# Kernel tuning notes

Hardware: AMD Instinct MI355X
Metric: run time of the kernel (lower is better)

Reference implementation:

```python
import jax, jax.numpy as jnp
import numpy as np

FFT_BINS = 513   # win_length//2 + 1
WIN = 1024       # win_length
H = 128          # LSTM hidden size (both blocks)
ENC = 256        # encoder_size
EPS = 1e-7


def _lstm_cell(x, h, c, Wih, Whh, bih, bhh):
    # x: [1, in], h/c: [1, H]; PyTorch gate order i, f, g, o
    g = x @ Wih.T + bih + h @ Whh.T + bhh
    i, f, gg, o = jnp.split(g, 4, axis=-1)
    c2 = jax.nn.sigmoid(f) * c + jax.nn.sigmoid(i) * jnp.tanh(gg)
    h2 = jax.nn.sigmoid(o) * jnp.tanh(c2)
    return h2, c2


def _sep_block(x, states, Wih0, Whh0, bih0, bhh0, Wih1, Whh1, bih1, bhh1, dw, db):
    # x: [1,1,in]; states: [1,1,2*2*H] -> [2(h/c), 2(layers), 1, H]
    st = states.reshape(2, 2, 1, H)
    h0, c0 = st[0], st[1]
    xt = x[:, 0]                                   # [1, in]
    h1, c1 = _lstm_cell(xt, h0[0], c0[0], Wih0, Whh0, bih0, bhh0)
    h2, c2 = _lstm_cell(h1, h0[1], c0[1], Wih1, Whh1, bih1, bhh1)
    mask = jax.nn.sigmoid(h2 @ dw.T + db)[:, None, :]   # [1,1,in]
    out_states = jnp.stack([jnp.stack([h1, h2]), jnp.stack([c1, c2])]).reshape(1, 1, -1)
    return mask, out_states


def setup_inputs() -> dict:
    key = jax.random.key(0)
    ks = jax.random.split(key, 32)
    s = 0.08  # ~ 1/sqrt(H), matching PyTorch LSTM init scale
    def n(i, shape, sc=s):
        return jax.random.normal(ks[i], shape, dtype=jnp.float32) * sc
    inp = {
        "mag": jax.random.uniform(ks[0], (1, 1, FFT_BINS), dtype=jnp.float32),
        "phase": n(1, (1, 1, FFT_BINS), 3.0),
        "in_states1": n(2, (1, 1, 2 * 2 * H), 1.0),
        "in_states2": n(3, (1, 1, 2 * 2 * H), 1.0),
        # sep1 LSTM (input 513)
        "w_ih1_0": n(4, (4 * H, FFT_BINS)), "w_hh1_0": n(5, (4 * H, H)),
        "b_ih1_0": n(6, (4 * H,)), "b_hh1_0": n(7, (4 * H,)),
        "w_ih1_1": n(8, (4 * H, H)), "w_hh1_1": n(9, (4 * H, H)),
        "b_ih1_1": n(10, (4 * H,)), "b_hh1_1": n(11, (4 * H,)),
        "dense1_w": n(12, (FFT_BINS, H)), "dense1_b": n(13, (FFT_BINS,)),
        # encoder 1x1 conv (no bias) + instant layernorm
        "enc_w": n(14, (ENC, WIN)),
        "gamma": jnp.ones((1, 1, ENC), jnp.float32),
        "beta": jnp.zeros((1, 1, ENC), jnp.float32),
        # sep2 LSTM (input 256)
        "w_ih2_0": n(15, (4 * H, ENC)), "w_hh2_0": n(16, (4 * H, H)),
        "b_ih2_0": n(17, (4 * H,)), "b_hh2_0": n(18, (4 * H,)),
        "w_ih2_1": n(19, (4 * H, H)), "w_hh2_1": n(20, (4 * H, H)),
        "b_ih2_1": n(21, (4 * H,)), "b_hh2_1": n(22, (4 * H,)),
        "dense2_w": n(23, (ENC, H)), "dense2_b": n(24, (ENC,)),
        # decoder 1x1 conv (no bias)
        "dec_w": n(25, (WIN, ENC)),
    }
    return inp


def reference(mag, phase, in_states1, in_states2,
              w_ih1_0, w_hh1_0, b_ih1_0, b_hh1_0,
              w_ih1_1, w_hh1_1, b_ih1_1, b_hh1_1,
              dense1_w, dense1_b, enc_w, gamma, beta,
              w_ih2_0, w_hh2_0, b_ih2_0, b_hh2_0,
              w_ih2_1, w_hh2_1, b_ih2_1, b_hh2_1,
              dense2_w, dense2_b, dec_w):
    # Branch 1: magnitude masking in STFT domain
    mask1, out_states1 = _sep_block(mag, in_states1, w_ih1_0, w_hh1_0, b_ih1_0,
                                    b_hh1_0, w_ih1_1, w_hh1_1, b_ih1_1, b_hh1_1,
                                    dense1_w, dense1_b)
    est_mag = mask1 * mag
    s1_stft = est_mag * jnp.exp(1j * phase)          # [1,1,513] complex64
    y1 = jnp.fft.irfft(s1_stft, axis=-1)             # [1,1,1024]
    # encoder 1x1 conv (permute + conv1d(k=1) == matmul over channels)
    enc = jnp.einsum('btw,ew->bte', y1, enc_w)       # [1,1,256]
    # instant layer norm over channels
    mean = jnp.mean(enc, axis=-1, keepdims=True)
    var = jnp.mean(jnp.square(enc - mean), axis=-1, keepdims=True)
    enc_norm = (enc - mean) / jnp.sqrt(var + EPS) * gamma + beta
    # Branch 2: learned-domain masking
    mask2, out_states2 = _sep_block(enc_norm, in_states2, w_ih2_0, w_hh2_0,
                                    b_ih2_0, b_hh2_0, w_ih2_1, w_hh2_1,
                                    b_ih2_1, b_hh2_1, dense2_w, dense2_b)
    est_enc = mask2 * enc
    decoded = jnp.einsum('bte,we->bwt', est_enc, dec_w)  # [1,1024,1]
    return decoded, out_states1, out_states2
```

## Files before the change

### kernel.cpp

```cpp
#include <hip/hip_runtime.h>
#include <hip/hip_bf16.h>


#define HDIM 128
#define NB 64
typedef __hip_bfloat16 bf16;

__device__ float G[4608];
#define O_H1A 0
#define O_H2A 128
#define O_C1A 256
#define O_C2A 384
#define O_H1B 512
#define O_H2B 640
#define O_C1B 768
#define O_C2B 896
#define O_XR  1024
#define O_XI  1600
#define O_Y   2176
#define O_ENC 3200
#define O_EST 3456

__device__ unsigned bar_cnt = 0;
__device__ unsigned bar_sense = 0;

__device__ __forceinline__ void gsync() {
    __syncthreads();
    if (threadIdx.x == 0) {
        unsigned s0 = __hip_atomic_load(&bar_sense, __ATOMIC_RELAXED, __HIP_MEMORY_SCOPE_AGENT);
        unsigned old = __hip_atomic_fetch_add(&bar_cnt, 1u, __ATOMIC_RELAXED, __HIP_MEMORY_SCOPE_AGENT);
        if (old == NB - 1) {
            __hip_atomic_store(&bar_cnt, 0u, __ATOMIC_RELAXED, __HIP_MEMORY_SCOPE_AGENT);
            __hip_atomic_store(&bar_sense, s0 + 1u, __ATOMIC_RELEASE, __HIP_MEMORY_SCOPE_AGENT);
        } else {
            while (__hip_atomic_load(&bar_sense, __ATOMIC_RELAXED, __HIP_MEMORY_SCOPE_AGENT) == s0)
                __builtin_amdgcn_s_sleep(2);
        }
    }
    __syncthreads();
}

__device__ __forceinline__ void gput(int i, float v) {
    __hip_atomic_store(&G[i], v, __ATOMIC_RELAXED, __HIP_MEMORY_SCOPE_AGENT);
}
__device__ __forceinline__ float gget(int i) {
    return __hip_atomic_load(&G[i], __ATOMIC_RELAXED, __HIP_MEMORY_SCOPE_AGENT);
}

__device__ __forceinline__ bool is_bf(const void* probe) {
    return (((const unsigned*)probe)[0] & 0xFFFFu) == 0x3F80u;
}
__device__ __forceinline__ float blo(unsigned u) { return __uint_as_float(u << 16); }
__device__ __forceinline__ float bhi(unsigned u) { return __uint_as_float(u & 0xFFFF0000u); }

template <bool BF>
__device__ __forceinline__ float ld1(const void* p, int i) {
    if (BF) return __uint_as_float((unsigned)((const unsigned short*)p)[i] << 16);
    return ((const float*)p)[i];
}
template <bool BF>
__device__ __forceinline__ float2 ld2(const void* p, int i) {
    if (BF) { unsigned u = ((const unsigned*)p)[i]; return float2{blo(u), bhi(u)}; }
    return ((const float2*)p)[i];
}
template <bool BF>
__device__ __forceinline__ float4 ld4(const void* p, int i) {
    if (BF) { uint2 u = ((const uint2*)p)[i]; return float4{blo(u.x), bhi(u.x), blo(u.y), bhi(u.y)}; }
    return ((const float4*)p)[i];
}
template <bool BF>
__device__ __forceinline__ void stout(void* p, int i, float v) {
    if (BF) ((bf16*)p)[i] = __float2bfloat16(v);
    else    ((float*)p)[i] = v;
}
__device__ __forceinline__ float wred(float v) {
#pragma unroll
    for (int m = 32; m; m >>= 1) v += __shfl_xor(v, m);
    return v;
}
__device__ __forceinline__ float sigm(float x) { return 1.f / (1.f + expf(-x)); }

struct P { const void* in[28]; void* out; };

template <bool BF>
__device__ __forceinline__ void body(const P& p, float* sA, float* sB, float* sR)
{
    const int tid = threadIdx.x, lane = tid & 63, wave = tid >> 6;
    const int b = blockIdx.x;
    const int gw = b * 4 + wave;

    { float2 v = ld2<BF>(p.in[0], tid); sA[2 * tid] = v.x; sA[2 * tid + 1] = v.y; }
    if (tid == 0) sA[512] = ld1<BF>(p.in[0], 512);
    if (tid < 64) { float2 v = ld2<BF>(p.in[2], tid); sB[2 * tid] = v.x; sB[2 * tid + 1] = v.y; }
    __syncthreads();
#pragma unroll
    for (int u = 0; u < 2; ++u) {
        const int row = wave * 128 + 2 * b + u;
        float acc = 0.f;
#pragma unroll
        for (int jj = 0; jj < 9; ++jj) {
            int k = lane + 64 * jj;
            if (k < 513) acc += ld1<BF>(p.in[4], row * 513 + k) * sA[k];
        }
        { float2 w2 = ld2<BF>(p.in[5], row * 64 + lane);
          acc += w2.x * sB[2 * lane] + w2.y * sB[2 * lane + 1]; }
        acc = wred(acc);
        if (lane == 0) sR[u * 4 + wave] = acc + ld1<BF>(p.in[6], row) + ld1<BF>(p.in[7], row);
    }
    __syncthreads();
    if (tid < 2) {
        int j = 2 * b + tid;
        float cin = ld1<BF>(p.in[2], 256 + j);
        float c2 = sigm(sR[tid * 4 + 1]) * cin + sigm(sR[tid * 4 + 0]) * tanhf(sR[tid * 4 + 2]);
        float h2 = sigm(sR[tid * 4 + 3]) * tanhf(c2);
        gput(O_H1A + j, h2); gput(O_C1A + j, c2);
    }
    gsync();

    if (tid < 128) sA[tid] = gget(O_H1A + tid);
    if (tid < 64) { float2 v = ld2<BF>(p.in[2], 64 + tid); sB[2 * tid] = v.x; sB[2 * tid + 1] = v.y; }
    __syncthreads();
#pragma unroll
    for (int u = 0; u < 2; ++u) {
        const int row = wave * 128 + 2 * b + u;
        float2 w2 = ld2<BF>(p.in[8], row * 64 + lane);
        float acc = w2.x * sA[2 * lane] + w2.y * sA[2 * lane + 1];
        float2 h2v = ld2<BF>(p.in[9], row * 64 + lane);
        acc += h2v.x * sB[2 * lane] + h2v.y * sB[2 * lane + 1];
        acc = wred(acc);
        if (lane == 0) sR[u * 4 + wave] = acc + ld1<BF>(p.in[10], row) + ld1<BF>(p.in[11], row);
    }
    __syncthreads();
    if (tid < 2) {
        int j = 2 * b + tid;
        float cin = ld1<BF>(p.in[2], 384 + j);
        float c2 = sigm(sR[tid * 4 + 1]) * cin + sigm(sR[tid * 4 + 0]) * tanhf(sR[tid * 4 + 2]);
        float h2 = sigm(sR[tid * 4 + 3]) * tanhf(c2);
        gput(O_H2A + j, h2); gput(O_C2A + j, c2);
    }
    gsync();

    if (tid < 128) sB[tid] = gget(O_H2A + tid);
    __syncthreads();
#pragma unroll
    for (int rep = 0; rep < 3; ++rep) {
        int g = b * 8 + wave * 2 + rep;
        if (rep < 2 || g == 512) {
            float2 w2 = ld2<BF>(p.in[12], g * 64 + lane);
            float acc = w2.x * sB[2 * lane] + w2.y * sB[2 * lane + 1];
            acc = wred(acc);
            if (lane == 0) {
                float m = sigm(acc + ld1<BF>(p.in[13], g));
                float em = m * ld1<BF>(p.in[0], g);
                float ph = ld1<BF>(p.in[1], g);
                float sp, cp; sincosf(ph, &sp, &cp);
                gput(O_XR + g, em * cp);
                gput(O_XI + g, em * sp);
            }
        }
    }
    if (b == 0)
        for (int t = tid; t < 512; t += 256) stout<BF>(p.out, 1024 + t, gget(t));
    gsync();

    for (int i = tid; i < 513; i += 256) { sA[i] = gget(O_XR + i); sB[i] = gget(O_XI + i); }
    __syncthreads();
#pragma unroll
    for (int rep = 0; rep < 2; ++rep) {
        const int n = b * 8 + wave * 2 + rep;
        float a1 = 0.f, a2 = 0.f;
#pragma unroll
        for (int jj = 0; jj < 9; ++jj) {
            int k = lane + 64 * jj;
            if (k < 513) {
                float t;
                if (k == 0) t = sA[0];
                else if (k == 512) t = (n & 1) ? -sA[512] : sA[512];
                else {
                    int m = (k * n) & 1023;
                    float th = (float)m * (6.283185307179586f / 1024.f);
                    float sn, cs; sincosf(th, &sn, &cs);
                    t = 2.f * (sA[k] * cs - sB[k] * sn);
                }
                a1 += t;
                a2 += (k & 1) ? -t : t;
            }
        }
        a1 = wred(a1); a2 = wred(a2);
        if (lane == 0) {
            gput(O_Y + n, a1 * (1.f / 1024.f));
            gput(O_Y + n + 512, a2 * (1.f / 1024.f));
        }
    }
    gsync();

    for (int i = tid; i < 1024; i += 256) sA[i] = gget(O_Y + i);
    __syncthreads();
    {
        float acc = 0.f;
#pragma unroll
        for (int q = 0; q < 4; ++q) {
            float4 w4 = ld4<BF>(p.in[14], gw * 256 + q * 64 + lane);
            const float* x4 = sA + q * 256 + 4 * lane;
            acc += w4.x * x4[0] + w4.y * x4[1] + w4.z * x4[2] + w4.w * x4[3];
        }
        acc = wred(acc);
        if (lane == 0) gput(O_ENC + gw, acc);
    }
    gsync();

    {
        float v = gget(O_ENC + tid);
        float s = wred(v);
        if (lane == 0) sR[8 + wave] = s;
        __syncthreads();
        float mean = (sR[8] + sR[9] + sR[10] + sR[11]) * (1.f / 256.f);
        __syncthreads();
        float d = v - mean;
        float s2 = wred(d * d);
        if (lane == 0) sR[8 + wave] = s2;
        __syncthreads();
        float var = (sR[8] + sR[9] + sR[10] + sR[11]) * (1.f / 256.f);
        float rs = rsqrtf(var + 1e-7f);
        sA[tid] = d * rs * ld1<BF>(p.in[15], tid) + ld1<BF>(p.in[16], tid);
        if (tid < 64) { float2 v2 = ld2<BF>(p.in[3], tid); sB[2 * tid] = v2.x; sB[2 * tid + 1] = v2.y; }
        __syncthreads();
#pragma unroll
        for (int u = 0; u < 2; ++u) {
            const int row = wave * 128 + 2 * b + u;
            float4 w4 = ld4<BF>(p.in[17], row * 64 + lane);
            const float* x4 = sA + 4 * lane;
            float acc = w4.x * x4[0] + w4.y * x4[1] + w4.z * x4[2] + w4.w * x4[3];
            float2 h2v = ld2<BF>(p.in[18], row * 64 + lane);
            acc += h2v.x * sB[2 * lane] + h2v.y * sB[2 * lane + 1];
            acc = wred(acc);
            if (lane == 0) sR[u * 4 + wave] = acc + ld1<BF>(p.in[19], row) + ld1<BF>(p.in[20], row);
        }
        __syncthreads();
        if (tid < 2) {
            int j = 2 * b + tid;
            float cin = ld1<BF>(p.in[3], 256 + j);
            float c2 = sigm(sR[tid * 4 + 1]) * cin + sigm(sR[tid * 4 + 0]) * tanhf(sR[tid * 4 + 2]);
            float h2 = sigm(sR[tid * 4 + 3]) * tanhf(c2);
            gput(O_H1B + j, h2); gput(O_C1B + j, c2);
        }
    }
    gsync();

    if (tid < 128) sA[tid] = gget(O_H1B + tid);
    if (tid < 64) { float2 v2 = ld2<BF>(p.in[3], 64 + tid); sB[2 * tid] = v2.x; sB[2 * tid + 1] = v2.y; }
    __syncthreads();
#pragma unroll
    for (int u = 0; u < 2; ++u) {
        const int row = wave * 128 + 2 * b + u;
        float2 w2 = ld2<BF>(p.in[21], row * 64 + lane);
        float acc = w2.x * sA[2 * lane] + w2.y * sA[2 * lane + 1];
        float2 h2v = ld2<BF>(p.in[22], row * 64 + lane);
        acc += h2v.x * sB[2 * lane] + h2v.y * sB[2 * lane + 1];
        acc = wred(acc);
        if (lane == 0) sR[u * 4 + wave] = acc + ld1<BF>(p.in[23], row) + ld1<BF>(p.in[24], row);
    }
    __syncthreads();
    if (tid < 2) {
        int j = 2 * b + tid;
        float cin = ld1<BF>(p.in[3], 384 + j);
        float c2 = sigm(sR[tid * 4 + 1]) * cin + sigm(sR[tid * 4 + 0]) * tanhf(sR[tid * 4 + 2]);
        float h2 = sigm(sR[tid * 4 + 3]) * tanhf(c2);
        gput(O_H2B + j, h2); gput(O_C2B + j, c2);
    }
    gsync();

    if (tid < 128) sB[tid] = gget(O_H2B + tid);
    __syncthreads();
    {
        float2 w2 = ld2<BF>(p.in[25], gw * 64 + lane);
        float acc = w2.x * sB[2 * lane] + w2.y * sB[2 * lane + 1];
        acc = wred(acc);
        if (lane == 0) {
            float m = sigm(acc + ld1<BF>(p.in[26], gw));
            gput(O_EST + gw, m * gget(O_ENC + gw));
        }
    }
    if (b == 0)
        for (int t = tid; t < 512; t += 256) stout<BF>(p.out, 1536 + t, gget(512 + t));
    gsync();

    sA[tid] = gget(O_EST + tid);
    __syncthreads();
#pragma unroll
    for (int rep = 0; rep < 4; ++rep) {
        int w = b * 16 + wave * 4 + rep;
        float4 w4 = ld4<BF>(p.in[27], w * 64 + lane);
        const float* x4 = sA + 4 * lane;
        float acc = w4.x * x4[0] + w4.y * x4[1] + w4.z * x4[2] + w4.w * x4[3];
        acc = wred(acc);
        if (lane == 0) stout<BF>(p.out, w, acc);
    }
}

__global__ __launch_bounds__(256, 1) void dtln_fused(P p)
{
    __shared__ float sA[1024];
    __shared__ float sB[516];
    __shared__ float sR[16];
    if (is_bf(p.in[15])) body<true>(p, sA, sB, sR);
    else                 body<false>(p, sA, sB, sR);
}

extern "C" void kernel_launch(void* const* d_in, const int* in_sizes, int n_in,
                              void* d_out, int out_size, void* d_ws, size_t ws_size,
                              hipStream_t stream)
{
    P p;
    for (int i = 0; i < 28; ++i) p.in[i] = d_in[i];
    p.out = d_out;
    dtln_fused<<<dim3(NB), dim3(256), 0, stream>>>(p);
}
```

Measured before the change: 165.7 us.

## Use 16 blocks of 1024 threads and drop final grid barrier via redundant mask

Reshapes the persistent fused kernel from 64 blocks of 256 threads to 16 blocks of 1024 threads, so fewer blocks take part in each software grid barrier. Every block now recomputes the full 256-element second dense mask locally, which removes the last grid sync and the global scratch round-trip before the decoder matmul. It also shortens the barrier spin sleep. The cost is redundant dense2 work in every block and less spread of the weight loads across compute units.

Measured after the change: 161.3 us. 2.7% less time.

```diff
diff --git a/kernel.cpp b/kernel.cpp
--- a/kernel.cpp
+++ b/kernel.cpp
@@ -3,7 +3,8 @@
 
 
 #define HDIM 128
-#define NB 64
+#define NB 16
+#define NT 1024
 typedef __hip_bfloat16 bf16;
 
 __device__ float G[4608];
@@ -19,7 +20,6 @@
 #define O_XI  1600
 #define O_Y   2176
 #define O_ENC 3200
-#define O_EST 3456
 
 __device__ unsigned bar_cnt = 0;
 __device__ unsigned bar_sense = 0;
@@ -34,7 +34,7 @@
             __hip_atomic_store(&bar_sense, s0 + 1u, __ATOMIC_RELEASE, __HIP_MEMORY_SCOPE_AGENT);
         } else {
             while (__hip_atomic_load(&bar_sense, __ATOMIC_RELAXED, __HIP_MEMORY_SCOPE_AGENT) == s0)
-                __builtin_amdgcn_s_sleep(2);
+                __builtin_amdgcn_s_sleep(1);
         }
     }
     __syncthreads();
@@ -87,32 +87,34 @@
 {
     const int tid = threadIdx.x, lane = tid & 63, wave = tid >> 6;
     const int b = blockIdx.x;
-    const int gw = b * 4 + wave;
-
-    { float2 v = ld2<BF>(p.in[0], tid); sA[2 * tid] = v.x; sA[2 * tid + 1] = v.y; }
-    if (tid == 0) sA[512] = ld1<BF>(p.in[0], 512);
+    const int gw = b * 16 + wave;
+    const int g4i = wave & 3;
+    const int slot = wave >> 2;
+
+    for (int i = tid; i < 513; i += NT) sA[i] = ld1<BF>(p.in[0], i);
     if (tid < 64) { float2 v = ld2<BF>(p.in[2], tid); sB[2 * tid] = v.x; sB[2 * tid + 1] = v.y; }
     __syncthreads();
 #pragma unroll
     for (int u = 0; u < 2; ++u) {
-        const int row = wave * 128 + 2 * b + u;
+        const int slotu = slot + 4 * u;
+        const int row = g4i * 128 + 8 * b + slotu;
         float acc = 0.f;
 #pragma unroll
         for (int jj = 0; jj < 9; ++jj) {
             int k = lane + 64 * jj;
             if (k < 513) acc += ld1<BF>(p.in[4], row * 513 + k) * sA[k];
         }
-        { float2 w2 = ld2<BF>(p.in[5], row * 64 + lane);
-          acc += w2.x * sB[2 * lane] + w2.y * sB[2 * lane + 1]; }
-        acc = wred(acc);
-        if (lane == 0) sR[u * 4 + wave] = acc + ld1<BF>(p.in[6], row) + ld1<BF>(p.in[7], row);
-    }
-    __syncthreads();
-    if (tid < 2) {
-        int j = 2 * b + tid;
+        float2 wh = ld2<BF>(p.in[5], row * 64 + lane);
+        acc += wh.x * sB[2 * lane] + wh.y * sB[2 * lane + 1];
+        acc = wred(acc);
+        if (lane == 0) sR[g4i * 8 + slotu] = acc + ld1<BF>(p.in[6], row) + ld1<BF>(p.in[7], row);
+    }
+    __syncthreads();
+    if (tid < 8) {
+        int j = 8 * b + tid;
         float cin = ld1<BF>(p.in[2], 256 + j);
-        float c2 = sigm(sR[tid * 4 + 1]) * cin + sigm(sR[tid * 4 + 0]) * tanhf(sR[tid * 4 + 2]);
-        float h2 = sigm(sR[tid * 4 + 3]) * tanhf(c2);
+        float c2 = sigm(sR[8 + tid]) * cin + sigm(sR[tid]) * tanhf(sR[16 + tid]);
+        float h2 = sigm(sR[24 + tid]) * tanhf(c2);
         gput(O_H1A + j, h2); gput(O_C1A + j, c2);
     }
     gsync();
@@ -122,20 +124,21 @@
     __syncthreads();
 #pragma unroll
     for (int u = 0; u < 2; ++u) {
-        const int row = wave * 128 + 2 * b + u;
-        float2 w2 = ld2<BF>(p.in[8], row * 64 + lane);
-        float acc = w2.x * sA[2 * lane] + w2.y * sA[2 * lane + 1];
-        float2 h2v = ld2<BF>(p.in[9], row * 64 + lane);
-        acc += h2v.x * sB[2 * lane] + h2v.y * sB[2 * lane + 1];
-        acc = wred(acc);
-        if (lane == 0) sR[u * 4 + wave] = acc + ld1<BF>(p.in[10], row) + ld1<BF>(p.in[11], row);
-    }
-    __syncthreads();
-    if (tid < 2) {
-        int j = 2 * b + tid;
+        const int slotu = slot + 4 * u;
+        const int row = g4i * 128 + 8 * b + slotu;
+        float2 wx = ld2<BF>(p.in[8], row * 64 + lane);
+        float acc = wx.x * sA[2 * lane] + wx.y * sA[2 * lane + 1];
+        float2 wh = ld2<BF>(p.in[9], row * 64 + lane);
+        acc += wh.x * sB[2 * lane] + wh.y * sB[2 * lane + 1];
+        acc = wred(acc);
+        if (lane == 0) sR[g4i * 8 + slotu] = acc + ld1<BF>(p.in[10], row) + ld1<BF>(p.in[11], row);
+    }
+    __syncthreads();
+    if (tid < 8) {
+        int j = 8 * b + tid;
         float cin = ld1<BF>(p.in[2], 384 + j);
-        float c2 = sigm(sR[tid * 4 + 1]) * cin + sigm(sR[tid * 4 + 0]) * tanhf(sR[tid * 4 + 2]);
-        float h2 = sigm(sR[tid * 4 + 3]) * tanhf(c2);
+        float c2 = sigm(sR[8 + tid]) * cin + sigm(sR[tid]) * tanhf(sR[16 + tid]);
+        float h2 = sigm(sR[24 + tid]) * tanhf(c2);
         gput(O_H2A + j, h2); gput(O_C2A + j, c2);
     }
     gsync();
@@ -144,8 +147,8 @@
     __syncthreads();
 #pragma unroll
     for (int rep = 0; rep < 3; ++rep) {
-        int g = b * 8 + wave * 2 + rep;
-        if (rep < 2 || g == 512) {
+        int g = gw + 256 * rep;
+        if (g < 513) {
             float2 w2 = ld2<BF>(p.in[12], g * 64 + lane);
             float acc = w2.x * sB[2 * lane] + w2.y * sB[2 * lane + 1];
             acc = wred(acc);
@@ -160,14 +163,14 @@
         }
     }
     if (b == 0)
-        for (int t = tid; t < 512; t += 256) stout<BF>(p.out, 1024 + t, gget(t));
-    gsync();
-
-    for (int i = tid; i < 513; i += 256) { sA[i] = gget(O_XR + i); sB[i] = gget(O_XI + i); }
+        for (int t = tid; t < 512; t += NT) stout<BF>(p.out, 1024 + t, gget(t));
+    gsync();
+
+    for (int i = tid; i < 513; i += NT) { sA[i] = gget(O_XR + i); sB[i] = gget(O_XI + i); }
     __syncthreads();
 #pragma unroll
     for (int rep = 0; rep < 2; ++rep) {
-        const int n = b * 8 + wave * 2 + rep;
+        const int n = 2 * gw + rep;
         float a1 = 0.f, a2 = 0.f;
 #pragma unroll
         for (int jj = 0; jj < 9; ++jj) {
@@ -194,7 +197,7 @@
     }
     gsync();
 
-    for (int i = tid; i < 1024; i += 256) sA[i] = gget(O_Y + i);
+    for (int i = tid; i < 1024; i += NT) sA[i] = gget(O_Y + i);
     __syncthreads();
     {
         float acc = 0.f;
@@ -210,38 +213,39 @@
     gsync();
 
     {
-        float v = gget(O_ENC + tid);
+        float v = (tid < 256) ? gget(O_ENC + tid) : 0.f;
         float s = wred(v);
-        if (lane == 0) sR[8 + wave] = s;
-        __syncthreads();
-        float mean = (sR[8] + sR[9] + sR[10] + sR[11]) * (1.f / 256.f);
+        if (lane == 0 && wave < 4) sR[40 + wave] = s;
+        __syncthreads();
+        float mean = (sR[40] + sR[41] + sR[42] + sR[43]) * (1.f / 256.f);
         __syncthreads();
         float d = v - mean;
         float s2 = wred(d * d);
-        if (lane == 0) sR[8 + wave] = s2;
-        __syncthreads();
-        float var = (sR[8] + sR[9] + sR[10] + sR[11]) * (1.f / 256.f);
+        if (lane == 0 && wave < 4) sR[40 + wave] = s2;
+        __syncthreads();
+        float var = (sR[40] + sR[41] + sR[42] + sR[43]) * (1.f / 256.f);
         float rs = rsqrtf(var + 1e-7f);
-        sA[tid] = d * rs * ld1<BF>(p.in[15], tid) + ld1<BF>(p.in[16], tid);
+        if (tid < 256) sA[tid] = d * rs * ld1<BF>(p.in[15], tid) + ld1<BF>(p.in[16], tid);
         if (tid < 64) { float2 v2 = ld2<BF>(p.in[3], tid); sB[2 * tid] = v2.x; sB[2 * tid + 1] = v2.y; }
         __syncthreads();
 #pragma unroll
         for (int u = 0; u < 2; ++u) {
-            const int row = wave * 128 + 2 * b + u;
+            const int slotu = slot + 4 * u;
+            const int row = g4i * 128 + 8 * b + slotu;
             float4 w4 = ld4<BF>(p.in[17], row * 64 + lane);
             const float* x4 = sA + 4 * lane;
             float acc = w4.x * x4[0] + w4.y * x4[1] + w4.z * x4[2] + w4.w * x4[3];
-            float2 h2v = ld2<BF>(p.in[18], row * 64 + lane);
-            acc += h2v.x * sB[2 * lane] + h2v.y * sB[2 * lane + 1];
+            float2 wh = ld2<BF>(p.in[18], row * 64 + lane);
+            acc += wh.x * sB[2 * lane] + wh.y * sB[2 * lane + 1];
             acc = wred(acc);
-            if (lane == 0) sR[u * 4 + wave] = acc + ld1<BF>(p.in[19], row) + ld1<BF>(p.in[20], row);
-        }
-        __syncthreads();
-        if (tid < 2) {
-            int j = 2 * b + tid;
+            if (lane == 0) sR[g4i * 8 + slotu] = acc + ld1<BF>(p.in[19], row) + ld1<BF>(p.in[20], row);
+        }
+        __syncthreads();
+        if (tid < 8) {
+            int j = 8 * b + tid;
             float cin = ld1<BF>(p.in[3], 256 + j);
-            float c2 = sigm(sR[tid * 4 + 1]) * cin + sigm(sR[tid * 4 + 0]) * tanhf(sR[tid * 4 + 2]);
-            float h2 = sigm(sR[tid * 4 + 3]) * tanhf(c2);
+            float c2 = sigm(sR[8 + tid]) * cin + sigm(sR[tid]) * tanhf(sR[16 + tid]);
+            float h2 = sigm(sR[24 + tid]) * tanhf(c2);
             gput(O_H1B + j, h2); gput(O_C1B + j, c2);
         }
     }
@@ -252,44 +256,45 @@
     __syncthreads();
 #pragma unroll
     for (int u = 0; u < 2; ++u) {
-        const int row = wave * 128 + 2 * b + u;
-        float2 w2 = ld2<BF>(p.in[21], row * 64 + lane);
-        float acc = w2.x * sA[2 * lane] + w2.y * sA[2 * lane + 1];
-        float2 h2v = ld2<BF>(p.in[22], row * 64 + lane);
-        acc += h2v.x * sB[2 * lane] + h2v.y * sB[2 * lane + 1];
-        acc = wred(acc);
-        if (lane == 0) sR[u * 4 + wave] = acc + ld1<BF>(p.in[23], row) + ld1<BF>(p.in[24], row);
-    }
-    __syncthreads();
-    if (tid < 2) {
-        int j = 2 * b + tid;
+        const int slotu = slot + 4 * u;
+        const int row = g4i * 128 + 8 * b + slotu;
+        float2 wx = ld2<BF>(p.in[21], row * 64 + lane);
+        float acc = wx.x * sA[2 * lane] + wx.y * sA[2 * lane + 1];
+        float2 wh = ld2<BF>(p.in[22], row * 64 + lane);
+        acc += wh.x * sB[2 * lane] + wh.y * sB[2 * lane + 1];
+        acc = wred(acc);
+        if (lane == 0) sR[g4i * 8 + slotu] = acc + ld1<BF>(p.in[23], row) + ld1<BF>(p.in[24], row);
+    }
+    __syncthreads();
+    if (tid < 8) {
+        int j = 8 * b + tid;
         float cin = ld1<BF>(p.in[3], 384 + j);
-        float c2 = sigm(sR[tid * 4 + 1]) * cin + sigm(sR[tid * 4 + 0]) * tanhf(sR[tid * 4 + 2]);
-        float h2 = sigm(sR[tid * 4 + 3]) * tanhf(c2);
+        float c2 = sigm(sR[8 + tid]) * cin + sigm(sR[tid]) * tanhf(sR[16 + tid]);
+        float h2 = sigm(sR[24 + tid]) * tanhf(c2);
         gput(O_H2B + j, h2); gput(O_C2B + j, c2);
     }
     gsync();
 
     if (tid < 128) sB[tid] = gget(O_H2B + tid);
-    __syncthreads();
-    {
-        float2 w2 = ld2<BF>(p.in[25], gw * 64 + lane);
+    if (tid >= 256 && tid < 512) sA[256 + (tid - 256)] = gget(O_ENC + (tid - 256));
+    __syncthreads();
+#pragma unroll
+    for (int r = 0; r < 16; ++r) {
+        const int e = wave * 16 + r;
+        float2 w2 = ld2<BF>(p.in[25], e * 64 + lane);
         float acc = w2.x * sB[2 * lane] + w2.y * sB[2 * lane + 1];
         acc = wred(acc);
         if (lane == 0) {
-            float m = sigm(acc + ld1<BF>(p.in[26], gw));
-            gput(O_EST + gw, m * gget(O_ENC + gw));
+            float m = sigm(acc + ld1<BF>(p.in[26], e));
+            sA[e] = m * sA[256 + e];
         }
     }
     if (b == 0)
-        for (int t = tid; t < 512; t += 256) stout<BF>(p.out, 1536 + t, gget(512 + t));
-    gsync();
-
-    sA[tid] = gget(O_EST + tid);
+        for (int t = tid; t < 512; t += NT) stout<BF>(p.out, 1536 + t, gget(512 + t));
     __syncthreads();
 #pragma unroll
     for (int rep = 0; rep < 4; ++rep) {
-        int w = b * 16 + wave * 4 + rep;
+        const int w = gw * 4 + rep;
         float4 w4 = ld4<BF>(p.in[27], w * 64 + lane);
         const float* x4 = sA + 4 * lane;
         float acc = w4.x * x4[0] + w4.y * x4[1] + w4.z * x4[2] + w4.w * x4[3];
@@ -298,11 +303,11 @@
     }
 }
 
-__global__ __launch_bounds__(256, 1) void dtln_fused(P p)
+__global__ __launch_bounds__(NT, 1) void dtln_fused(P p)
 {
     __shared__ float sA[1024];
     __shared__ float sB[516];
-    __shared__ float sR[16];
+    __shared__ float sR[48];
     if (is_bf(p.in[15])) body<true>(p, sA, sB, sR);
     else                 body<false>(p, sA, sB, sR);
 }
@@ -314,5 +319,5 @@
     P p;
     for (int i = 0; i < 28; ++i) p.in[i] = d_in[i];
     p.out = d_out;
-    dtln_fused<<<dim3(NB), dim3(256), 0, stream>>>(p);
-}
+    dtln_fused<<<dim3(NB), dim3(NT), 0, stream>>>(p);
+}
```
